# Performance work log

Hardware: AMD Instinct MI355X
Metric: run time of the kernel (lower is better)

## Reference

```python
import jax, jax.numpy as jnp
import numpy as np
from jax import lax

D = 1024      # d_model
L = 2048      # seq_len
B = 2         # batch
DS = 16       # d_state
DC = 4        # d_conv
DI = 2 * D    # d_inner (expand=2)
DTR = D // 16 # dt_rank = ceil(d_model/16)
ETA = 0.1     # Hebbian learning rate
DECAY = 0.95  # Hebbian state decay
EPS = 1e-5


def rmsnorm(x, w):
    return x * lax.rsqrt(jnp.mean(x * x, axis=-1, keepdims=True) + EPS) * w


def setup_inputs() -> dict:
    key = jax.random.key(0)
    ks = jax.random.split(key, 14)
    s = 0.02
    x = jax.random.normal(ks[0], (B, L, D), jnp.float32)
    norm_w = jnp.ones((D,), jnp.float32)
    in_proj_w = jax.random.normal(ks[1], (2 * DI, D), jnp.float32) * s
    conv_w = jax.random.normal(ks[2], (DI, 1, DC), jnp.float32) * s
    conv_b = jnp.zeros((DI,), jnp.float32)
    x_proj_w = jax.random.normal(ks[3], (DTR + 2 * DS, DI), jnp.float32) * s
    dt_proj_w = jax.random.normal(ks[4], (DI, DTR), jnp.float32) * (DTR ** -0.5)
    dt_init = jax.random.uniform(ks[5], (DI,), jnp.float32, 1e-3, 0.1)
    dt_proj_b = jnp.log(jnp.expm1(dt_init))  # inverse softplus
    A_log = jnp.log(jnp.broadcast_to(jnp.arange(1, DS + 1, dtype=jnp.float32), (DI, DS)))
    D_param = jnp.ones((DI,), jnp.float32)
    out_proj_w = jax.random.normal(ks[6], (D, DI), jnp.float32) * s
    norm_hebb_w = jnp.ones((D,), jnp.float32)
    Wk = jax.random.normal(ks[7], (D, D), jnp.float32) * (D ** -0.5)
    Wv = jax.random.normal(ks[8], (D, D), jnp.float32) * (D ** -0.5)
    return {"x": x, "norm_w": norm_w, "in_proj_w": in_proj_w, "conv_w": conv_w,
            "conv_b": conv_b, "x_proj_w": x_proj_w, "dt_proj_w": dt_proj_w,
            "dt_proj_b": dt_proj_b, "A_log": A_log, "D_param": D_param,
            "out_proj_w": out_proj_w, "norm_hebb_w": norm_hebb_w, "Wk": Wk, "Wv": Wv}


def _mamba(x, in_proj_w, conv_w, conv_b, x_proj_w, dt_proj_w, dt_proj_b,
           A_log, D_param, out_proj_w):
    xz = jnp.einsum('bld,ed->ble', x, in_proj_w)        # [B,L,2*DI]
    xm, z = jnp.split(xz, 2, axis=-1)
    # depthwise causal conv over time
    xc = jnp.transpose(xm, (0, 2, 1))                    # [B,DI,L]
    xc = lax.conv_general_dilated(xc, conv_w, (1,), [(DC - 1, 0)],
                                  feature_group_count=DI,
                                  dimension_numbers=('NCH', 'OIH', 'NCH'))
    xc = xc + conv_b[None, :, None]
    u = jax.nn.silu(jnp.transpose(xc, (0, 2, 1)))        # [B,L,DI]
    x_dbl = jnp.einsum('bld,ed->ble', u, x_proj_w)       # [B,L,DTR+2*DS]
    dt, Bm, Cm = jnp.split(x_dbl, [DTR, DTR + DS], axis=-1)
    dt = jax.nn.softplus(jnp.einsum('blr,dr->bld', dt, dt_proj_w) + dt_proj_b)  # [B,L,DI]
    A = -jnp.exp(A_log)                                   # [DI,DS]

    def step(h, inp):
        dt_t, B_t, C_t, u_t = inp                         # [B,DI],[B,DS],[B,DS],[B,DI]
        h = h * jnp.exp(dt_t[..., None] * A) + (dt_t * u_t)[..., None] * B_t[:, None, :]
        y_t = jnp.einsum('bds,bs->bd', h, C_t)
        return h, y_t

    xs = (dt.transpose(1, 0, 2), Bm.transpose(1, 0, 2),
          Cm.transpose(1, 0, 2), u.transpose(1, 0, 2))
    h0 = jnp.zeros((B, DI, DS), x.dtype)
    _, ys = lax.scan(step, h0, xs)                        # ys: [L,B,DI]
    y = ys.transpose(1, 0, 2) + u * D_param
    y = y * jax.nn.silu(z)
    return jnp.einsum('ble,de->bld', y, out_proj_w)


def _hebbian(xn, Wk, Wv):
    # M_t = DECAY*M_{t-1} + ETA * k_t v_t^T ; read y_t = x_t @ M_{t-1}, M_0 = 0
    # => y_t = ETA * sum_{s<t} DECAY^{t-1-s} (x_t . k_s) v_s  (decayed causal linear attn)
    k = jnp.einsum('bld,de->ble', xn, Wk)
    v = jnp.einsum('bld,de->ble', xn, Wv)
    t = jnp.arange(L)[:, None]
    s = jnp.arange(L)[None, :]
    mask = s < t
    Wts = jnp.where(mask, DECAY ** jnp.maximum(t - 1 - s, 0).astype(xn.dtype), 0.0)
    scores = jnp.einsum('btd,bsd->bts', xn, k) * Wts      # [B,L,L]
    y = ETA * jnp.einsum('bts,bse->bte', scores, v)
    return y


def reference(x, norm_w, in_proj_w, conv_w, conv_b, x_proj_w, dt_proj_w,
              dt_proj_b, A_log, D_param, out_proj_w, norm_hebb_w, Wk, Wv):
    residual = x
    h = rmsnorm(x, norm_w)
    h = _mamba(h, in_proj_w, conv_w, conv_b, x_proj_w, dt_proj_w, dt_proj_b,
               A_log, D_param, out_proj_w)
    x2 = residual + h
    xn = rmsnorm(x2, norm_hebb_w)
    y = _hebbian(xn, Wk, Wv)
    return x2 + y
```

## Files before the change

### kernel.cpp

```cpp
#include <hip/hip_runtime.h>
#include <hip/hip_bf16.h>
#include <math.h>

#define D_MODEL 1024
#define SEQ_L   2048
#define BATCH   2
#define NSTATE  16
#define DCONV   4
#define DINNER  2048
#define DTRANK  64
#define ETA_C   0.1f
#define DECAY_C 0.95f
#define EPS_C   1e-5f
#define MTOK    (BATCH*SEQ_L)
#define LOG2_DECAY (-0.07400058144377693f)

typedef unsigned short u16;
typedef __attribute__((ext_vector_type(8))) short bf16x8;
typedef __attribute__((ext_vector_type(4))) float f32x4;

__device__ inline u16 f2b(float f) {
    __hip_bfloat16 h = __float2bfloat16(f);
    return *reinterpret_cast<u16*>(&h);
}
__device__ inline float b2f(u16 u) {
    unsigned int x = ((unsigned int)u) << 16;
    return __uint_as_float(x);
}
__device__ inline float silu_f(float z) { return z / (1.0f + expf(-z)); }

#define GLL16(gsrc, ldst) \
    __builtin_amdgcn_global_load_lds((const __attribute__((address_space(1))) void*)(gsrc), \
                                     (__attribute__((address_space(3))) void*)(ldst), 16, 0, 0)

__global__ __launch_bounds__(256)
void rmsnorm_b_kernel(const float* __restrict__ in, const float* __restrict__ w,
                      u16* __restrict__ outb)
{
    int row = blockIdx.x;
    int t = threadIdx.x;
    const float4* ip = (const float4*)(in + (size_t)row * D_MODEL);
    float4 v = ip[t];
    float ss = v.x*v.x + v.y*v.y + v.z*v.z + v.w*v.w;
    #pragma unroll
    for (int m = 1; m < 64; m <<= 1) ss += __shfl_xor(ss, m);
    __shared__ float red[4];
    if ((t & 63) == 0) red[t >> 6] = ss;
    __syncthreads();
    float total = red[0] + red[1] + red[2] + red[3];
    float sc = rsqrtf(total * (1.0f / D_MODEL) + EPS_C);
    float4 wv = ((const float4*)w)[t];
    ushort4 o;
    o.x = f2b(v.x * sc * wv.x); o.y = f2b(v.y * sc * wv.y);
    o.z = f2b(v.z * sc * wv.z); o.w = f2b(v.w * sc * wv.w);
    ((ushort4*)(outb + (size_t)row * D_MODEL))[t] = o;
}

__global__ __launch_bounds__(256)
void cvt_bf16_kernel(const float* __restrict__ in, u16* __restrict__ out, int n4)
{
    int i = blockIdx.x * 256 + threadIdx.x;
    if (i >= n4) return;
    float4 v = *(const float4*)(in + (size_t)i * 4);
    ushort4 o; o.x = f2b(v.x); o.y = f2b(v.y); o.z = f2b(v.z); o.w = f2b(v.w);
    *(ushort4*)(out + (size_t)i * 4) = o;
}

__global__ __launch_bounds__(256)
void cvt_slice64_kernel(const float* __restrict__ in, u16* __restrict__ out)
{
    int i = blockIdx.x * 256 + threadIdx.x;
    int row = i >> 4, c4 = (i & 15) << 2;
    float4 v = *(const float4*)(in + (size_t)row * 96 + c4);
    ushort4 o; o.x = f2b(v.x); o.y = f2b(v.y); o.z = f2b(v.z); o.w = f2b(v.w);
    *(ushort4*)(out + (size_t)row * 64 + c4) = o;
}

__device__ inline u16 to_b16(float v) { return f2b(v); }
__device__ inline u16 to_b16(u16 v)   { return v; }

template<typename TIN>
__global__ __launch_bounds__(256)
void transpose_b16_kernel(const TIN* __restrict__ in, u16* __restrict__ outT,
                          int ldIn, int ldOut, long long sIn, long long sOut)
{
    __shared__ u16 tile[32][34];
    in   += (size_t)blockIdx.z * sIn;
    outT += (size_t)blockIdx.z * sOut;
    int c0 = blockIdx.x * 32, r0 = blockIdx.y * 32;
    int tx = threadIdx.x & 31, ty = threadIdx.x >> 5;
    #pragma unroll
    for (int i = 0; i < 4; ++i)
        tile[ty + 8*i][tx] = to_b16(in[(size_t)(r0 + ty + 8*i) * ldIn + c0 + tx]);
    __syncthreads();
    #pragma unroll
    for (int i = 0; i < 4; ++i)
        outT[(size_t)(c0 + ty + 8*i) * ldOut + r0 + tx] = tile[tx][ty + 8*i];
}

__global__ __launch_bounds__(256)
void conv_silu_kernel(const u16* __restrict__ xzb, const float* __restrict__ cw,
                      const float* __restrict__ cb, float* __restrict__ u)
{
    int i4 = blockIdx.x * 256 + threadIdx.x;
    int d4 = (i4 & 511) << 2;
    int row = i4 >> 9;
    int l = row & (SEQ_L - 1);
    const u16* base = xzb + (size_t)row * (2*DINNER) + d4;
    float4 cbv = *(const float4*)(cb + d4);
    float s[4] = {cbv.x, cbv.y, cbv.z, cbv.w};
    float4 w0 = *(const float4*)(cw + (d4+0)*DCONV);
    float4 w1 = *(const float4*)(cw + (d4+1)*DCONV);
    float4 w2 = *(const float4*)(cw + (d4+2)*DCONV);
    float4 w3 = *(const float4*)(cw + (d4+3)*DCONV);
    const float* wj[4] = {(const float*)&w0, (const float*)&w1,
                          (const float*)&w2, (const float*)&w3};
    #pragma unroll
    for (int j = 0; j < DCONV; ++j) {
        int lj = l - (DCONV-1) + j;
        if (lj >= 0) {
            ushort4 xv = *(const ushort4*)(base + (size_t)(lj - l) * (2*DINNER));
            s[0] = fmaf(wj[0][j], b2f(xv.x), s[0]);
            s[1] = fmaf(wj[1][j], b2f(xv.y), s[1]);
            s[2] = fmaf(wj[2][j], b2f(xv.z), s[2]);
            s[3] = fmaf(wj[3][j], b2f(xv.w), s[3]);
        }
    }
    float4 o;
    o.x = s[0] / (1.0f + expf(-s[0]));
    o.y = s[1] / (1.0f + expf(-s[1]));
    o.z = s[2] / (1.0f + expf(-s[2]));
    o.w = s[3] / (1.0f + expf(-s[3]));
    *(float4*)(u + (size_t)i4 * 4) = o;
}

#define NCHUNK 64
#define CHLEN  32

__global__ __launch_bounds__(256)
void scanA_kernel(const float* __restrict__ dt, const float* __restrict__ u,
                  const float* __restrict__ xdbl, const float* __restrict__ A_log,
                  float2* __restrict__ PC)
{
    int b = blockIdx.x >> 3;
    int d = ((blockIdx.x & 7) << 8) | threadIdx.x;
    int chunk = blockIdx.y;
    float Aa[NSTATE], Pv[NSTATE], cv[NSTATE];
    #pragma unroll
    for (int s = 0; s < NSTATE; ++s) {
        Aa[s] = -expf(A_log[d * NSTATE + s]);
        Pv[s] = 1.0f; cv[s] = 0.0f;
    }
    const float* dtp = dt + ((size_t)b * SEQ_L) * DINNER + d;
    const float* up  = u  + ((size_t)b * SEQ_L) * DINNER + d;
    const float* xdp = xdbl + (size_t)b * SEQ_L * 96 + DTRANK;
    int t0 = chunk * CHLEN;
    #pragma unroll 4
    for (int t = t0; t < t0 + CHLEN; ++t) {
        float dtv = dtp[(size_t)t * DINNER];
        float uv  = up [(size_t)t * DINNER];
        float du = dtv * uv;
        float Bv[NSTATE];
        *(float4*)&Bv[0]  = *(const float4*)(xdp + t * 96);
        *(float4*)&Bv[4]  = *(const float4*)(xdp + t * 96 + 4);
        *(float4*)&Bv[8]  = *(const float4*)(xdp + t * 96 + 8);
        *(float4*)&Bv[12] = *(const float4*)(xdp + t * 96 + 12);
        #pragma unroll
        for (int s = 0; s < NSTATE; ++s) {
            float e = __expf(dtv * Aa[s]);
            Pv[s] *= e;
            cv[s] = fmaf(cv[s], e, du * Bv[s]);
        }
    }
    #pragma unroll
    for (int s = 0; s < NSTATE; ++s) {
        size_t o = (((size_t)chunk * BATCH + b) * NSTATE + s) * DINNER + d;
        PC[o] = make_float2(Pv[s], cv[s]);
    }
}

__global__ __launch_bounds__(256)
void scanB_kernel(float2* __restrict__ PC)
{
    int flat = blockIdx.x * 256 + threadIdx.x;
    int d = flat & (DINNER - 1);
    int s = (flat >> 11) & (NSTATE - 1);
    int b = flat >> 15;
    float h = 0.0f;
    #pragma unroll
    for (int ch = 0; ch < NCHUNK; ++ch) {
        size_t o = (((size_t)ch * BATCH + b) * NSTATE + s) * DINNER + d;
        float2 pc = PC[o];
        PC[o].x = h;
        h = pc.x * h + pc.y;
    }
}

__global__ __launch_bounds__(256)
void scanC_gate_kernel(const float* __restrict__ dt, const float* __restrict__ u,
                       const float* __restrict__ xdbl, const float* __restrict__ A_log,
                       const float2* __restrict__ PC, const float* __restrict__ Dp,
                       const u16* __restrict__ xzb, u16* __restrict__ ybb)
{
    int b = blockIdx.x >> 3;
    int d = ((blockIdx.x & 7) << 8) | threadIdx.x;
    int chunk = blockIdx.y;
    float Aa[NSTATE], h[NSTATE];
    #pragma unroll
    for (int s = 0; s < NSTATE; ++s) {
        Aa[s] = -expf(A_log[d * NSTATE + s]);
        h[s] = PC[(((size_t)chunk * BATCH + b) * NSTATE + s) * DINNER + d].x;
    }
    float Dv = Dp[d];
    const float* dtp = dt + ((size_t)b * SEQ_L) * DINNER + d;
    const float* up  = u  + ((size_t)b * SEQ_L) * DINNER + d;
    const float* xdp = xdbl + (size_t)b * SEQ_L * 96 + DTRANK;
    const u16* zp = xzb + ((size_t)b * SEQ_L) * (2*DINNER) + DINNER + d;
    u16* yp = ybb + ((size_t)b * SEQ_L) * DINNER + d;
    int t0 = chunk * CHLEN;
    #pragma unroll 4
    for (int t = t0; t < t0 + CHLEN; ++t) {
        float dtv = dtp[(size_t)t * DINNER];
        float uv  = up [(size_t)t * DINNER];
        float du = dtv * uv;
        float Bv[NSTATE], Cv[NSTATE];
        *(float4*)&Bv[0]  = *(const float4*)(xdp + t * 96);
        *(float4*)&Bv[4]  = *(const float4*)(xdp + t * 96 + 4);
        *(float4*)&Bv[8]  = *(const float4*)(xdp + t * 96 + 8);
        *(float4*)&Bv[12] = *(const float4*)(xdp + t * 96 + 12);
        *(float4*)&Cv[0]  = *(const float4*)(xdp + t * 96 + 16);
        *(float4*)&Cv[4]  = *(const float4*)(xdp + t * 96 + 20);
        *(float4*)&Cv[8]  = *(const float4*)(xdp + t * 96 + 24);
        *(float4*)&Cv[12] = *(const float4*)(xdp + t * 96 + 28);
        float y = 0.0f;
        #pragma unroll
        for (int s = 0; s < NSTATE; ++s) {
            float e = __expf(dtv * Aa[s]);
            h[s] = fmaf(h[s], e, du * Bv[s]);
            y = fmaf(h[s], Cv[s], y);
        }
        float z = b2f(zp[(size_t)t * (2*DINNER)]);
        yp[(size_t)t * DINNER] = f2b((y + uv * Dv) * silu_f(z));
    }
}

#define BM 64
#define BN 64
#define BK 16

template<int TRANSB, int EPI>
__global__ __launch_bounds__(256)
void gemm_kernel(const float* __restrict__ A, int lda,
                 const float* __restrict__ B, int ldb,
                 float* __restrict__ C, int ldc,
                 int M, int N, int Kc, const float* __restrict__ bias,
                 long long sCz)
{
    __shared__ float As[BK][BM + 4];
    __shared__ float Bs[BK][BN + 4];
    C += (size_t)blockIdx.z * sCz;
    int kOff = blockIdx.z * Kc;
    int m0 = blockIdx.y * BM, n0 = blockIdx.x * BN;
    int t = threadIdx.x;
    int tx = t & 15, ty = t >> 4;
    int rA = t >> 2, c4 = (t & 3) << 2;
    float acc[4][4] = {};
    for (int k0 = kOff; k0 < kOff + Kc; k0 += BK) {
        float4 av = make_float4(0.f,0.f,0.f,0.f);
        if (m0 + rA < M) av = *(const float4*)(A + (size_t)(m0 + rA) * lda + k0 + c4);
        As[c4+0][rA] = av.x; As[c4+1][rA] = av.y; As[c4+2][rA] = av.z; As[c4+3][rA] = av.w;
        float4 bv = make_float4(0.f,0.f,0.f,0.f);
        if (n0 + rA < N) bv = *(const float4*)(B + (size_t)(n0 + rA) * ldb + k0 + c4);
        Bs[c4+0][rA] = bv.x; Bs[c4+1][rA] = bv.y; Bs[c4+2][rA] = bv.z; Bs[c4+3][rA] = bv.w;
        __syncthreads();
        #pragma unroll
        for (int kk = 0; kk < BK; ++kk) {
            float4 a4 = *(const float4*)&As[kk][ty << 2];
            float4 b4 = *(const float4*)&Bs[kk][tx << 2];
            float a[4] = {a4.x, a4.y, a4.z, a4.w};
            float b[4] = {b4.x, b4.y, b4.z, b4.w};
            #pragma unroll
            for (int i = 0; i < 4; ++i)
                #pragma unroll
                for (int j = 0; j < 4; ++j)
                    acc[i][j] = fmaf(a[i], b[j], acc[i][j]);
        }
        __syncthreads();
    }
    #pragma unroll
    for (int i = 0; i < 4; ++i) {
        int m = m0 + (ty << 2) + i;
        if (m >= M) continue;
        #pragma unroll
        for (int j = 0; j < 4; ++j) {
            int n = n0 + (tx << 2) + j;
            if (n >= N) continue;
            float v = acc[i][j];
            if (EPI == 1) {
                float xv = v + bias[n];
                v = fmaxf(xv, 0.0f) + log1pf(expf(-fabsf(xv)));
            }
            C[(size_t)m * ldc + n] = v;
        }
    }
}

__global__ __launch_bounds__(256)
void reduce8_kernel(const float* __restrict__ p, float* __restrict__ o, int n)
{
    int i = blockIdx.x * 256 + threadIdx.x;
    if (i >= n) return;
    float s = 0.0f;
    #pragma unroll
    for (int z = 0; z < 8; ++z) s += p[(size_t)z * n + i];
    o[i] = s;
}

template<int EPI, int SWZ = 0, int TRI = 0>
__global__ __launch_bounds__(256)
void mfma_nt_kernel(const u16* __restrict__ A, int lda, long long sA,
                    const u16* __restrict__ B, int ldb, long long sB,
                    float* __restrict__ Cf, u16* __restrict__ Cb, int ldc, long long sC,
                    int K, const float* __restrict__ Src)
{
    __shared__ u16 As[128 * 64];
    __shared__ u16 Bs[128 * 64];
    int bz = blockIdx.z;
    A += (size_t)bz * sA; B += (size_t)bz * sB;
    if (EPI == 1 || EPI == 3) Cb += (size_t)bz * sC; else Cf += (size_t)bz * sC;
    if (EPI == 2) Src += (size_t)bz * sC;
    int bx = blockIdx.x, by = blockIdx.y;
    if (SWZ) {
        int gx = gridDim.x;
        int nwg = gx * gridDim.y;
        int flat = by * gx + bx;
        int swz = (flat & 7) * (nwg >> 3) + (flat >> 3);
        bx = swz % gx; by = swz / gx;
    }
    int m0 = by * 128, n0 = bx * 128;
    if (TRI == 1 && n0 > m0) return;
    int t = threadIdx.x;
    int lane = t & 63, w = t >> 6;
    int wm = (w >> 1) * 64, wn = (w & 1) * 64;
    int l15 = lane & 15, lhi = lane >> 4;

    int lrow = lane >> 3;
    int scol = ((lane & 7) ^ lrow) << 3;

    f32x4 acc[4][4] = {};
    int Keff = (TRI == 2) ? (m0 + 128 < K ? m0 + 128 : K) : K;
    const int nk = Keff >> 6;

    for (int kt = 0; kt < nk; ++kt) {
        int kb = kt << 6;
        #pragma unroll
        for (int q = 0; q < 4; ++q) {
            int c = (q << 2) + w;
            int row = (c << 3) + lrow;
            GLL16(A + (size_t)(m0 + row) * lda + kb + scol, &As[c << 9]);
            GLL16(B + (size_t)(n0 + row) * ldb + kb + scol, &Bs[c << 9]);
        }
        __syncthreads();
        #pragma unroll
        for (int ks = 0; ks < 2; ++ks) {
            int csw = (ks * 32 + lhi * 8) ^ ((l15 & 7) << 3);
            bf16x8 af[4], bfr[4];
            #pragma unroll
            for (int f = 0; f < 4; ++f) {
                af[f]  = *(const bf16x8*)&As[(wm + f*16 + l15) * 64 + csw];
                bfr[f] = *(const bf16x8*)&Bs[(wn + f*16 + l15) * 64 + csw];
            }
            #pragma unroll
            for (int i = 0; i < 4; ++i)
                #pragma unroll
                for (int j = 0; j < 4; ++j)
                    acc[i][j] = __builtin_amdgcn_mfma_f32_16x16x32_bf16(
                                    af[i], bfr[j], acc[i][j], 0, 0, 0);
        }
        __syncthreads();
    }
    int rb0 = m0 + wm + lhi * 4;
    int cb0 = n0 + wn + l15;
    #pragma unroll
    for (int mf = 0; mf < 4; ++mf) {
        #pragma unroll
        for (int nf = 0; nf < 4; ++nf) {
            #pragma unroll
            for (int i = 0; i < 4; ++i) {
                int r = rb0 + mf * 16 + i;
                int cc = cb0 + nf * 16;
                float v = acc[mf][nf][i];
                if (EPI == 0) {
                    Cf[(size_t)r * ldc + cc] = v;
                } else if (EPI == 1) {
                    Cb[(size_t)r * ldc + cc] = f2b(v);
                } else if (EPI == 2) {
                    Cf[(size_t)r * ldc + cc] = Src[(size_t)r * ldc + cc] + v;
                } else if (EPI == 4) {
                    float xv = v + Src[cc];
                    Cf[(size_t)r * ldc + cc] = fmaxf(xv, 0.0f) + log1pf(expf(-fabsf(xv)));
                } else {
                    float wv = (cc < r) ? ETA_C * exp2f((float)(r - 1 - cc) * LOG2_DECAY) : 0.0f;
                    Cb[(size_t)r * ldc + cc] = f2b(v * wv);
                }
            }
        }
    }
}

extern "C" void kernel_launch(void* const* d_in, const int* in_sizes, int n_in,
                              void* d_out, int out_size, void* d_ws, size_t ws_size,
                              hipStream_t stream)
{
    const float* x        = (const float*)d_in[0];
    const float* norm_w   = (const float*)d_in[1];
    const float* in_proj  = (const float*)d_in[2];
    const float* conv_w   = (const float*)d_in[3];
    const float* conv_b   = (const float*)d_in[4];
    const float* x_proj   = (const float*)d_in[5];
    const float* dt_projw = (const float*)d_in[6];
    const float* dt_projb = (const float*)d_in[7];
    const float* A_log    = (const float*)d_in[8];
    const float* D_param  = (const float*)d_in[9];
    const float* out_proj = (const float*)d_in[10];
    const float* hebb_w   = (const float*)d_in[11];
    const float* Wk       = (const float*)d_in[12];
    const float* Wv       = (const float*)d_in[13];
    float* out = (float*)d_out;

    float* ws = (float*)d_ws;
    const size_t M1 = 1024 * 1024;
    u16*   xnb  = (u16*)ws;
    u16*   opb  = (u16*)ws;
    u16*   xzb  = (u16*)(ws + 2*M1);
    u16*   xnb2 = (u16*)(ws + 2*M1);
    u16*   kvb16= (u16*)(ws + 4*M1);
    u16*   vT16 = (u16*)(ws + 8*M1);
    float2* PCbuf = (float2*)(ws + 10*M1);
    u16*   scb16= (u16*)(ws + 10*M1);
    u16*   wkvT = (u16*)(ws + 14*M1);
    float* ubuf = ws + 18*M1;
    float* xdbl = ws + 26*M1;
    float* dtb  = ws + 26*M1 + M1/2;
    u16*   ipb  = (u16*)dtb;
    float* pbuf = ws + 34*M1 + M1/2;
    u16*   xdb16 = (u16*)(ws + 34*M1 + M1/2);
    u16*   dtw16 = (u16*)(ws + 34*M1 + M1/2 + 128*1024);
    u16*   ybb  = (u16*)(ws + 34*M1 + M1/2);
    size_t need = (40*M1 + M1/2) * sizeof(float);
    if (ws_size < need) return;

    dim3 blk(256);
    const long long LD  = (long long)SEQ_L * D_MODEL;
    const long long LL  = (long long)SEQ_L * SEQ_L;
    const int NXP = MTOK * 96;

    rmsnorm_b_kernel<<<MTOK, blk, 0, stream>>>(x, norm_w, xnb);
    cvt_bf16_kernel<<<(2*DINNER*D_MODEL/4 + 255)/256, blk, 0, stream>>>(in_proj, ipb, 2*DINNER*D_MODEL/4);
    mfma_nt_kernel<1><<<dim3(32, 32, 1), blk, 0, stream>>>(
        xnb, D_MODEL, 0, ipb, D_MODEL, 0, nullptr, xzb, 2*DINNER, 0, D_MODEL, nullptr);
    conv_silu_kernel<<<(MTOK*DINNER/4)/256, blk, 0, stream>>>(xzb, conv_w, conv_b, ubuf);
    gemm_kernel<1,0><<<dim3(2, MTOK/BM, 8), blk, 0, stream>>>(
        ubuf, DINNER, x_proj, DINNER, pbuf, 96, MTOK, 96, DINNER/8, nullptr, (long long)NXP);
    reduce8_kernel<<<(NXP + 255)/256, blk, 0, stream>>>(pbuf, xdbl, NXP);
    cvt_bf16_kernel<<<(DINNER*DTRANK/4 + 255)/256, blk, 0, stream>>>(dt_projw, dtw16, DINNER*DTRANK/4);
    cvt_slice64_kernel<<<(MTOK*16)/256, blk, 0, stream>>>(xdbl, xdb16);
    mfma_nt_kernel<4><<<dim3(DINNER/128, MTOK/128, 1), blk, 0, stream>>>(
        xdb16, DTRANK, 0, dtw16, DTRANK, 0, dtb, nullptr, DINNER, 0, DTRANK, dt_projb);
    scanA_kernel<<<dim3(16, NCHUNK), blk, 0, stream>>>(dtb, ubuf, xdbl, A_log, PCbuf);
    scanB_kernel<<<256, blk, 0, stream>>>(PCbuf);
    scanC_gate_kernel<<<dim3(16, NCHUNK), blk, 0, stream>>>(
        dtb, ubuf, xdbl, A_log, PCbuf, D_param, xzb, ybb);
    cvt_bf16_kernel<<<(D_MODEL*DINNER/4 + 255)/256, blk, 0, stream>>>(out_proj, opb, D_MODEL*DINNER/4);
    transpose_b16_kernel<float><<<dim3(32, 32, 1), blk, 0, stream>>>(Wk, wkvT, D_MODEL, D_MODEL, 0, 0);
    transpose_b16_kernel<float><<<dim3(32, 32, 1), blk, 0, stream>>>(Wv, wkvT + (size_t)D_MODEL*D_MODEL, D_MODEL, D_MODEL, 0, 0);
    mfma_nt_kernel<2><<<dim3(8, 32, 1), blk, 0, stream>>>(
        ybb, DINNER, 0, opb, DINNER, 0, out, nullptr, D_MODEL, 0, DINNER, x);
    rmsnorm_b_kernel<<<MTOK, blk, 0, stream>>>(out, hebb_w, xnb2);
    mfma_nt_kernel<1><<<dim3(16, 32, 1), blk, 0, stream>>>(
        xnb2, D_MODEL, 0, wkvT, D_MODEL, 0, nullptr, kvb16, 2*D_MODEL, 0, D_MODEL, nullptr);
    transpose_b16_kernel<u16><<<dim3(32, 64, BATCH), blk, 0, stream>>>(
        kvb16 + D_MODEL, vT16, 2*D_MODEL, SEQ_L, LL, LD);
    mfma_nt_kernel<3,0,1><<<dim3(16, 16, BATCH), blk, 0, stream>>>(
        xnb2, D_MODEL, LD, kvb16, 2*D_MODEL, LL, nullptr, scb16, SEQ_L, LL, D_MODEL, nullptr);
    mfma_nt_kernel<2,0,2><<<dim3(8, 16, BATCH), blk, 0, stream>>>(
        scb16, SEQ_L, LL, vT16, SEQ_L, LD, out, nullptr, D_MODEL, LD, SEQ_L, out);
}
```

Baseline: 399.6 us.

## Use 256x256 double-buffered 8-wave MFMA kernel for input projection GEMM

Replaces the 128x128 tile GEMM for the in_proj (4096x4096x1024) with a new 512-thread kernel using 256x256 tiles, double-buffered LDS, and a phased schedule that interleaves global-to-LDS loads with MFMA compute. Larger tiles raise data reuse per LDS load, and the prefetch overlap hides memory latency. It also removes the SWZ block remapping from the generic kernel. Costs are 128KB of LDS per block, which allows only one block per CU, and a 256-block grid that may underfill the GPU.

```diff
diff --git a/kernel.cpp b/kernel.cpp
--- a/kernel.cpp
+++ b/kernel.cpp
@@ -330,13 +330,6 @@
     if (EPI == 1 || EPI == 3) Cb += (size_t)bz * sC; else Cf += (size_t)bz * sC;
     if (EPI == 2) Src += (size_t)bz * sC;
     int bx = blockIdx.x, by = blockIdx.y;
-    if (SWZ) {
-        int gx = gridDim.x;
-        int nwg = gx * gridDim.y;
-        int flat = by * gx + bx;
-        int swz = (flat & 7) * (nwg >> 3) + (flat >> 3);
-        bx = swz % gx; by = swz / gx;
-    }
     int m0 = by * 128, n0 = bx * 128;
     if (TRI == 1 && n0 > m0) return;
     int t = threadIdx.x;
@@ -406,6 +399,114 @@
             }
         }
     }
+}
+
+__global__ __launch_bounds__(512)
+void mfma_nt8_kernel(const u16* __restrict__ A, int lda,
+                     const u16* __restrict__ B, int ldb,
+                     u16* __restrict__ Cb, int ldc, int K)
+{
+    __shared__ u16 As[2][256 * 64];
+    __shared__ u16 Bs[2][256 * 64];
+    int m0 = blockIdx.y * 256, n0 = blockIdx.x * 256;
+    int t = threadIdx.x;
+    int lane = t & 63, w = t >> 6;
+    int wr = w >> 2, wc = w & 3;
+    int l15 = lane & 15, lhi = lane >> 4;
+    int lrow = lane >> 3, lcol = lane & 7;
+    int scol = (lcol ^ lrow) << 3;
+
+    const int nk = K >> 6;
+    const int npair = nk >> 1;
+
+    f32x4 acc[8][4] = {};
+    bf16x8 bfr[4][2];
+
+#define SA8(bi, kt, q) GLL16(A + (size_t)(m0 + ((q)<<6) + (w<<3) + lrow)*lda + ((kt)<<6) + scol, \
+                             &As[bi][((((q)<<6) + (w<<3)) << 6)])
+#define SB8(bi, kt, q) GLL16(B + (size_t)(n0 + ((q)<<6) + (w<<3) + lrow)*ldb + ((kt)<<6) + scol, \
+                             &Bs[bi][((((q)<<6) + (w<<3)) << 6)])
+#define BAR8() __builtin_amdgcn_s_barrier()
+#define VMW8() asm volatile("s_waitcnt vmcnt(8)" ::: "memory")
+#define VMW0() asm volatile("s_waitcnt vmcnt(0)" ::: "memory")
+
+#define PHASE8(BI, Q, LB) do { \
+    bf16x8 af_[2][2]; \
+    _Pragma("unroll") for (int ks = 0; ks < 2; ++ks) { \
+        int csw = (ks*32 + lhi*8) ^ ((l15 & 7) << 3); \
+        if (LB) { _Pragma("unroll") for (int nf = 0; nf < 4; ++nf) \
+            bfr[nf][ks] = *(const bf16x8*)&Bs[BI][((wc<<6) + nf*16 + l15)*64 + csw]; } \
+        _Pragma("unroll") for (int mi = 0; mi < 2; ++mi) \
+            af_[mi][ks] = *(const bf16x8*)&As[BI][((wr<<7) + ((Q)*2+mi)*16 + l15)*64 + csw]; \
+    } \
+    __builtin_amdgcn_s_setprio(1); \
+    _Pragma("unroll") for (int mi = 0; mi < 2; ++mi) \
+      _Pragma("unroll") for (int nf = 0; nf < 4; ++nf) \
+        _Pragma("unroll") for (int ks = 0; ks < 2; ++ks) \
+          acc[(Q)*2+mi][nf] = __builtin_amdgcn_mfma_f32_16x16x32_bf16( \
+              af_[mi][ks], bfr[nf][ks], acc[(Q)*2+mi][nf], 0, 0, 0); \
+    __builtin_amdgcn_s_setprio(0); \
+} while (0)
+
+    SB8(0,0,0); SB8(0,0,1); SB8(0,0,2); SB8(0,0,3);
+    SA8(0,0,0); SA8(0,0,1); SA8(0,0,2); SA8(0,0,3);
+    SB8(1,1,0); SB8(1,1,1); SB8(1,1,2); SB8(1,1,3);
+    SA8(1,1,0); SA8(1,1,2);
+
+    for (int pair = 0; pair < npair; ++pair) {
+        int k0 = pair << 1;
+        int k2 = k0 + 2, k3 = k0 + 3;
+        bool s2 = k2 < nk, s3 = k3 < nk;
+        SA8(1, k0+1, 1); SA8(1, k0+1, 3);
+        VMW8();
+        BAR8();
+        PHASE8(0, 0, true);
+        BAR8();
+        if (s2) { SB8(0, k2, 0); SB8(0, k2, 1); }
+        PHASE8(0, 1, false);
+        BAR8();
+        if (s2) { SB8(0, k2, 2); SB8(0, k2, 3); }
+        PHASE8(0, 2, false);
+        BAR8();
+        if (s2) { SA8(0, k2, 0); SA8(0, k2, 2); }
+        PHASE8(0, 3, false);
+        BAR8();
+        if (s2) { SA8(0, k2, 1); SA8(0, k2, 3); VMW8(); }
+        else    { VMW0(); }
+        BAR8();
+        PHASE8(1, 0, true);
+        BAR8();
+        if (s3) { SB8(1, k3, 0); SB8(1, k3, 1); }
+        PHASE8(1, 1, false);
+        BAR8();
+        if (s3) { SB8(1, k3, 2); SB8(1, k3, 3); }
+        PHASE8(1, 2, false);
+        BAR8();
+        if (s3) { SA8(1, k3, 0); SA8(1, k3, 2); }
+        PHASE8(1, 3, false);
+        BAR8();
+    }
+
+    int rb0 = m0 + (wr << 7) + lhi * 4;
+    int cb0 = n0 + (wc << 6) + l15;
+    #pragma unroll
+    for (int mf = 0; mf < 8; ++mf) {
+        #pragma unroll
+        for (int nf = 0; nf < 4; ++nf) {
+            #pragma unroll
+            for (int i = 0; i < 4; ++i) {
+                int r = rb0 + mf * 16 + i;
+                int cc = cb0 + nf * 16;
+                Cb[(size_t)r * ldc + cc] = f2b(acc[mf][nf][i]);
+            }
+        }
+    }
+#undef SA8
+#undef SB8
+#undef BAR8
+#undef VMW8
+#undef VMW0
+#undef PHASE8
 }
 
 extern "C" void kernel_launch(void* const* d_in, const int* in_sizes, int n_in,
@@ -457,8 +558,8 @@
 
     rmsnorm_b_kernel<<<MTOK, blk, 0, stream>>>(x, norm_w, xnb);
     cvt_bf16_kernel<<<(2*DINNER*D_MODEL/4 + 255)/256, blk, 0, stream>>>(in_proj, ipb, 2*DINNER*D_MODEL/4);
-    mfma_nt_kernel<1><<<dim3(32, 32, 1), blk, 0, stream>>>(
-        xnb, D_MODEL, 0, ipb, D_MODEL, 0, nullptr, xzb, 2*DINNER, 0, D_MODEL, nullptr);
+    mfma_nt8_kernel<<<dim3(16, 16), 512, 0, stream>>>(
+        xnb, D_MODEL, ipb, D_MODEL, xzb, 2*DINNER, D_MODEL);
     conv_silu_kernel<<<(MTOK*DINNER/4)/256, blk, 0, stream>>>(xzb, conv_w, conv_b, ubuf);
     gemm_kernel<1,0><<<dim3(2, MTOK/BM, 8), blk, 0, stream>>>(
         ubuf, DINNER, x_proj, DINNER, pbuf, 96, MTOK, 96, DINNER/8, nullptr, (long long)NXP);
```

Result: no change. 392.6 us (-1.7%).
